# Kernel optimization log

Hardware: AMD Instinct MI355X
Metric: run time of the kernel (lower is better)

The kernel has to match this reference:

```python
import jax, jax.numpy as jnp
import numpy as np
import math

DIM = 512
HEADS = 8
DIM_HEAD = DIM // HEADS
TIME_DIM = 512
EPS = 1e-5


def _ln(x, g, b):
    m = jnp.mean(x, axis=-1, keepdims=True)
    v = jnp.var(x, axis=-1, keepdims=True)
    return (x - m) * jax.lax.rsqrt(v + EPS) * g + b


def setup_inputs() -> dict:
    key = jax.random.key(0)
    ks = jax.random.split(key, 16)
    s = 0.02
    return {
        "con_features": jax.random.normal(ks[0], (4, 1024, DIM), jnp.float32),
        "diff_features": jax.random.normal(ks[1], (4, 1024, DIM), jnp.float32),
        "time_emb": jax.random.normal(ks[2], (4, TIME_DIM), jnp.float32),
        "ln_con_g": jnp.ones((DIM,), jnp.float32),
        "ln_con_b": jnp.zeros((DIM,), jnp.float32),
        "ln_diff_g": jnp.ones((DIM,), jnp.float32),
        "ln_diff_b": jnp.zeros((DIM,), jnp.float32),
        "wq": jax.random.normal(ks[3], (DIM, DIM), jnp.float32) * s,
        "wk": jax.random.normal(ks[4], (DIM, DIM), jnp.float32) * s,
        "wv": jax.random.normal(ks[5], (DIM, DIM), jnp.float32) * s,
        "w_out": jax.random.normal(ks[6], (DIM, DIM), jnp.float32) * s,
        "b_out": jnp.zeros((DIM,), jnp.float32),
        "w_emd1": jax.random.normal(ks[7], (TIME_DIM, 2 * DIM), jnp.float32) * s,
        "b_emd1": jnp.zeros((2 * DIM,), jnp.float32),
        "w_emd2": jax.random.normal(ks[8], (2 * DIM, 2 * DIM), jnp.float32) * s,
        "b_emd2": jnp.zeros((2 * DIM,), jnp.float32),
        "mlp_ln_g": jnp.ones((DIM,), jnp.float32),
        "mlp_ln_b": jnp.zeros((DIM,), jnp.float32),
        "mlp_w1": jax.random.normal(ks[9], (DIM, DIM), jnp.float32) * s,
        "mlp_b1": jnp.zeros((DIM,), jnp.float32),
        "mlp_w2": jax.random.normal(ks[10], (DIM, DIM), jnp.float32) * s,
        "mlp_b2": jnp.zeros((DIM,), jnp.float32),
    }


def reference(con_features, diff_features, time_emb,
              ln_con_g, ln_con_b, ln_diff_g, ln_diff_b,
              wq, wk, wv, w_out, b_out,
              w_emd1, b_emd1, w_emd2, b_emd2,
              mlp_ln_g, mlp_ln_b, mlp_w1, mlp_b1, mlp_w2, mlp_b2):
    b, n, _ = diff_features.shape
    fea_q = _ln(diff_features, ln_diff_g, ln_diff_b)
    fea_kv = _ln(con_features, ln_con_g, ln_con_b)
    # projections (no bias) + split heads: b n (h d) -> b h n d
    def heads(x):
        return x.reshape(b, n, HEADS, DIM_HEAD).transpose(0, 2, 1, 3)
    q = heads(fea_q @ wq)
    k = heads(fea_kv @ wk)
    v = heads(fea_kv @ wv)
    # 2D FFT over (n, d), ortho norm
    qf = jnp.fft.fft2(q, axes=(-2, -1), norm="ortho")
    kf = jnp.fft.fft2(k, axes=(-2, -1), norm="ortho")
    dots = jnp.einsum("bhnd,bhmd->bhnm", qf, jnp.conj(kf))  # q @ k^H
    attn_c = jnp.fft.ifft2(dots, axes=(-2, -1), norm="ortho")
    mag = jnp.sqrt(attn_c.real ** 2 + attn_c.imag ** 2)
    attn = jax.nn.softmax(mag, axis=-1) / math.sqrt(DIM_HEAD)
    out = jnp.einsum("bhnm,bhmd->bhnd", attn, v)
    out = out.transpose(0, 2, 1, 3).reshape(b, n, DIM)  # b h n d -> b n (h d)
    # global per-sample normalization over (n, dim); torch.std uses ddof=1
    mu = jnp.mean(out, axis=(-2, -1), keepdims=True)
    sd = jnp.std(out, axis=(-2, -1), keepdims=True, ddof=1)
    out1 = (out - mu) / sd
    # FiLM from time embedding
    t = jax.nn.silu(time_emb @ w_emd1 + b_emd1)
    t = t @ w_emd2 + b_emd2
    mean_t, std_t = jnp.split(t, 2, axis=-1)
    out1 = out1 * std_t[:, None, :] + mean_t[:, None, :]
    out1 = out1 @ w_out + b_out
    # FeedForward: LN -> Linear -> GELU(exact) -> Linear
    h = _ln(out1, mlp_ln_g, mlp_ln_b)
    h = jax.nn.gelu(h @ mlp_w1 + mlp_b1, approximate=False)
    return h @ mlp_w2 + mlp_b2
```

## Files before the change

kernel.cpp:

```cpp
#include <hip/hip_runtime.h>
#include <math.h>


typedef _Float16 f16;
typedef _Float16 f16x4 __attribute__((ext_vector_type(4)));
typedef _Float16 f16x8 __attribute__((ext_vector_type(8)));
typedef float f32x4 __attribute__((ext_vector_type(4)));

#define ROWS 4096
#define NTOK 1024
#define NB   4
#define NH   8
#define DH   64

__device__ __forceinline__ void glds16(const f16* g, f16* l) {
    __builtin_amdgcn_global_load_lds((const __attribute__((address_space(1))) void*)g,
                                     (__attribute__((address_space(3))) void*)l, 16, 0, 0);
}

struct PrepArgs { const float* src[6]; f16* dst[6]; };

__device__ __forceinline__ void ln_row(const float* __restrict__ x, const float* __restrict__ g,
                                       const float* __restrict__ bb, f16* __restrict__ o, int lane) {
    float v[8]; float s = 0.f;
#pragma unroll
    for (int j = 0; j < 8; j++) { v[j] = x[lane + 64 * j]; s += v[j]; }
#pragma unroll
    for (int d = 32; d >= 1; d >>= 1) s += __shfl_xor(s, d, 64);
    float mean = s * (1.f / 512.f);
    float q = 0.f;
#pragma unroll
    for (int j = 0; j < 8; j++) { float t = v[j] - mean; q += t * t; }
#pragma unroll
    for (int d = 32; d >= 1; d >>= 1) q += __shfl_xor(q, d, 64);
    float inv = rsqrtf(q * (1.f / 512.f) + 1e-5f);
#pragma unroll
    for (int j = 0; j < 8; j++) {
        int c = lane + 64 * j;
        o[c] = (f16)((v[j] - mean) * inv * g[c] + bb[c]);
    }
}

__global__ __launch_bounds__(256) void k_pre(PrepArgs pa, float* statsp,
                                             const float* __restrict__ b_emd1, const float* __restrict__ b_emd2,
                                             float* __restrict__ tbacc, float* __restrict__ filmp,
                                             float* __restrict__ rstats,
                                             const float* __restrict__ diff, const float* __restrict__ g_dif,
                                             const float* __restrict__ b_dif, f16* __restrict__ A16,
                                             const float* __restrict__ con, const float* __restrict__ g_con,
                                             const float* __restrict__ b_con, f16* __restrict__ C16) {
    __shared__ float smem[1056];
    const int id = blockIdx.x, tid = threadIdx.x;
    if (id < 16) {
        int o = id * 256 + tid;
        tbacc[o] = b_emd1[o & 1023];
        filmp[o] = b_emd2[o & 1023];
        if (id < 4) statsp[id * 256 + tid] = 0.f;
    } else if (id < 48) {
        rstats[(id - 16) * 256 + tid] = 0.f;
    } else if (id < 1584) {
        int pid = id - 48;
        int m = pid >> 8, rem = pid & 255;
        int o0 = (rem & 15) * 32, i0 = (rem >> 4) * 32;
        int tx = tid & 31, ty = tid >> 5;
        const float* src = pa.src[m];
        f16* dst = pa.dst[m];
        for (int r = ty; r < 32; r += 8)
            smem[r * 33 + tx] = src[(i0 + r) * 512 + o0 + tx];
        __syncthreads();
        for (int r = ty; r < 32; r += 8)
            dst[(o0 + r) * 512 + i0 + tx] = (f16)smem[tx * 33 + r];
    } else {
        int lane = tid & 63, wid = tid >> 6;
        long row = (long)(id - 1584) * 4 + wid;
        if (row < ROWS) ln_row(diff + row * 512, g_dif, b_dif, A16 + row * 512, lane);
        else { long r = row - ROWS; ln_row(con + r * 512, g_con, b_con, C16 + r * 512, lane); }
    }
}

__global__ __launch_bounds__(256) void k_qkv(const f16* __restrict__ A16, const f16* __restrict__ C16,
                                             const f16* __restrict__ wqT, const f16* __restrict__ wkT,
                                             const f16* __restrict__ wvT,
                                             f16* __restrict__ Qh, f16* __restrict__ Kf, f16* __restrict__ Vt,
                                             const float* __restrict__ temb, const float* __restrict__ w_emd1,
                                             float* __restrict__ tbacc) {
    __shared__ __attribute__((aligned(16))) f16 sh[128 * 128 + 64 * 128];
    const int id = blockIdx.x, tid = threadIdx.x;
    if (id >= 768) {
        float* tsh = (float*)sh;
        int pid = id - 768;
        int c = (pid & 3) * 256 + tid;
        int k0 = (pid >> 2) * 32;
        if (tid < 128) tsh[(tid >> 5) * 32 + (tid & 31)] = temb[(tid >> 5) * 512 + k0 + (tid & 31)];
        __syncthreads();
        float a0 = 0.f, a1 = 0.f, a2 = 0.f, a3 = 0.f;
#pragma unroll 8
        for (int k = 0; k < 32; k++) {
            float w = w_emd1[(k0 + k) * 1024 + c];
            a0 += tsh[k] * w; a1 += tsh[32 + k] * w; a2 += tsh[64 + k] * w; a3 += tsh[96 + k] * w;
        }
        atomicAdd(&tbacc[c], a0);        atomicAdd(&tbacc[1024 + c], a1);
        atomicAdd(&tbacc[2048 + c], a2); atomicAdd(&tbacc[3072 + c], a3);
        return;
    }
    f16* Ash = sh;
    f16* Bsh = sh + 128 * 128;
    const int z = id >> 8;
    const f16* A  = (z == 0) ? A16 : C16;
    const f16* BT = (z == 0) ? wqT : (z == 1) ? wkT : wvT;
    const int lane = tid & 63, wid = tid >> 6;
    const int quad = lane >> 4, l15 = lane & 15;
    const int m0 = (id & 31) * 128, n0 = ((id >> 5) & 7) * 64;
    const int wm = (wid >> 1) * 64, wn = (wid & 1) * 32;
    const int srow = lane >> 4, slot = lane & 15;
    f32x4 acc[4][2] = {};
    for (int kk = 0; kk < 512; kk += 128) {
        if (kk) __syncthreads();
#pragma unroll
        for (int c = 0; c < 8; c++) {
            int r = c * 16 + 4 * wid + srow;
            int j = slot ^ (r & 7);
            glds16(&A[(long)(m0 + r) * 512 + kk + 8 * j], &Ash[(c * 16 + 4 * wid) * 128]);
        }
#pragma unroll
        for (int c = 0; c < 4; c++) {
            int r = c * 16 + 4 * wid + srow;
            int j = slot ^ (r & 7);
            glds16(&BT[(long)(n0 + r) * 512 + kk + 8 * j], &Bsh[(c * 16 + 4 * wid) * 128]);
        }
        __syncthreads();
#pragma unroll
        for (int ks = 0; ks < 4; ks++) {
            const int rslot = ((ks * 4 + quad) ^ (l15 & 7)) * 8;
            f16x8 af[4], bf[2];
#pragma unroll
            for (int t = 0; t < 4; t++)
                af[t] = *(const f16x8*)&Ash[(wm + t * 16 + l15) * 128 + rslot];
#pragma unroll
            for (int t = 0; t < 2; t++)
                bf[t] = *(const f16x8*)&Bsh[(wn + t * 16 + l15) * 128 + rslot];
#pragma unroll
            for (int mt = 0; mt < 4; mt++)
#pragma unroll
                for (int nt = 0; nt < 2; nt++)
                    acc[mt][nt] = __builtin_amdgcn_mfma_f32_16x16x32_f16(af[mt], bf[nt], acc[mt][nt], 0, 0, 0);
        }
    }
    __syncthreads();
    const int bb = m0 >> 10, nn0 = m0 & 1023, h = (id >> 5) & 7;
    if (z <= 1) {
#pragma unroll
        for (int mt = 0; mt < 4; mt++)
#pragma unroll
            for (int nt = 0; nt < 2; nt++)
#pragma unroll
                for (int r = 0; r < 4; r++)
                    sh[(wm + mt * 16 + quad * 4 + r) * 72 + wn + nt * 16 + l15] = (f16)acc[mt][nt][r];
        __syncthreads();
        f16* dst = (z == 0) ? Qh : Kf;
        long basebh = ((long)(bb * NH + h)) * NTOK * DH;
#pragma unroll
        for (int q2 = 0; q2 < 4; q2++) {
            int c = tid + q2 * 256;
            int row = c >> 3, col = (c & 7) * 8;
            int n = nn0 + row;
            int nr = (z == 1) ? ((NTOK - n) & (NTOK - 1)) : n;
            *(f16x8*)&dst[basebh + (long)nr * DH + col] = *(const f16x8*)&sh[row * 72 + col];
        }
    } else {
#pragma unroll
        for (int mt = 0; mt < 4; mt++)
#pragma unroll
            for (int nt = 0; nt < 2; nt++)
#pragma unroll
                for (int r = 0; r < 4; r++)
                    sh[(wn + nt * 16 + l15) * 136 + wm + mt * 16 + quad * 4 + r] = (f16)acc[mt][nt][r];
        __syncthreads();
        long basev = ((long)(bb * NH + h)) * DH * NTOK;
#pragma unroll
        for (int q2 = 0; q2 < 4; q2++) {
            int c = tid + q2 * 256;
            int d = c >> 4, col = (c & 15) * 8;
            *(f16x8*)&Vt[basev + (long)d * NTOK + nn0 + col] = *(const f16x8*)&sh[d * 136 + col];
        }
    }
}

__global__ __launch_bounds__(256) void k_attn(const f16* __restrict__ Q, const f16* __restrict__ Kf,
                                              const f16* __restrict__ Vt,
                                              float* __restrict__ Opart, float* __restrict__ lpart) {
    __shared__ __attribute__((aligned(16))) f16 Ksh[128 * 64];
    __shared__ __attribute__((aligned(16))) f16 Vsh[64 * 128];
    __shared__ __attribute__((aligned(16))) f16 PshT[4 * 16 * 136];
    const int id = blockIdx.x, tid = threadIdx.x;
    const int lane = tid & 63, wid = tid >> 6;
    const int quad = lane >> 4, l15 = lane & 15;
    const int bh = id & 31;
    const int rest = id >> 5;
    const int qt = rest & 15, half = rest >> 4;
    const int b = bh >> 3, hh = bh & 7, q0 = qt * 64;
    const int kbase = half * 512;
    const f16* Qbh = Q + (long)bh * NTOK * DH;
    const f16* Kbh = Kf + (long)bh * NTOK * DH;
    const f16* Vbh = Vt + (long)bh * DH * NTOK;
    const int rl = lane >> 3, jj8 = (lane & 7) ^ rl;
    const int rl4 = lane >> 4, jjv = (lane & 15) ^ (4 * wid + rl4);
    const int qrow = q0 + wid * 16 + l15;
    f16x8 qf[2];
    qf[0] = *(const f16x8*)&Qbh[(long)qrow * DH + quad * 8];
    qf[1] = *(const f16x8*)&Qbh[(long)qrow * DH + 32 + quad * 8];
    f32x4 O[4] = {};
    float l_acc = 0.f;
    f16* Pw = PshT + wid * 16 * 136;

    for (int k0 = 0; k0 < 512; k0 += 128) {
        if (k0) __syncthreads();
        const int kb = kbase + k0;
#pragma unroll
        for (int c = 0; c < 4; c++) {
            int rk = c * 32 + 8 * wid + rl;
            glds16(&Kbh[(long)(kb + rk) * DH + 8 * jj8], &Ksh[(c * 32 + 8 * wid) * 64]);
        }
#pragma unroll
        for (int c = 0; c < 4; c++) {
            int rv = c * 16 + 4 * wid + rl4;
            glds16(&Vbh[(long)rv * NTOK + kb + 8 * jjv], &Vsh[(c * 16 + 4 * wid) * 128]);
        }
        __syncthreads();
        f32x4 st[8] = {};
#pragma unroll
        for (int ks = 0; ks < 2; ks++) {
            const int slot = ((ks * 4 + quad) ^ (l15 & 7)) * 8;
#pragma unroll
            for (int nt = 0; nt < 8; nt++) {
                f16x8 kf = *(const f16x8*)&Ksh[(nt * 16 + l15) * 64 + slot];
                st[nt] = __builtin_amdgcn_mfma_f32_16x16x32_f16(kf, qf[ks], st[nt], 0, 0, 0);
            }
        }
#pragma unroll
        for (int nt = 0; nt < 8; nt++) {
            float p0 = __expf(fminf(fabsf(st[nt][0]) - 8.f, 11.f));
            float p1 = __expf(fminf(fabsf(st[nt][1]) - 8.f, 11.f));
            float p2 = __expf(fminf(fabsf(st[nt][2]) - 8.f, 11.f));
            float p3 = __expf(fminf(fabsf(st[nt][3]) - 8.f, 11.f));
            l_acc += (p0 + p1) + (p2 + p3);
            f16x4 pk = { (f16)p0, (f16)p1, (f16)p2, (f16)p3 };
            *(f16x4*)&Pw[l15 * 136 + 16 * nt + quad * 4] = pk;
        }
#pragma unroll
        for (int ks = 0; ks < 4; ks++) {
            f16x8 pf = *(const f16x8*)&Pw[l15 * 136 + 32 * ks + quad * 8];
            const int vslot = ((ks * 4 + quad) ^ l15) * 8;
#pragma unroll
            for (int vt = 0; vt < 4; vt++) {
                f16x8 vf = *(const f16x8*)&Vsh[(vt * 16 + l15) * 128 + vslot];
                O[vt] = __builtin_amdgcn_mfma_f32_16x16x32_f16(pf, vf, O[vt], 0, 0, 0);
            }
        }
    }
    l_acc += __shfl_xor(l_acc, 16, 64);
    l_acc += __shfl_xor(l_acc, 32, 64);
    if (quad == 0) lpart[half * (32 * NTOK) + bh * NTOK + qrow] = l_acc;
    float* Od = Opart + (size_t)half * ROWS * 512;
#pragma unroll
    for (int t = 0; t < 4; t++)
#pragma unroll
        for (int r = 0; r < 4; r++) {
            int gn = q0 + wid * 16 + quad * 4 + r;
            int gc = hh * DH + t * 16 + l15;
            Od[((long)b * NTOK + gn) * 512 + gc] = O[t][r];
        }
}

__global__ __launch_bounds__(256) void k_comb(const float* __restrict__ Opart, const float* __restrict__ lpart,
                                              f16* __restrict__ aout16, float* __restrict__ statsp,
                                              const float* __restrict__ tbacc, const float* __restrict__ w_emd2,
                                              float* __restrict__ filmp) {
    __shared__ float tsh[128];
    __shared__ float rbuf[8];
    const int id = blockIdx.x, tid = threadIdx.x;
    if (id >= 2048) {
        int pid = id - 2048;
        int c = (pid & 3) * 256 + tid;
        int k0 = (pid >> 2) * 32;
        if (tid < 128) {
            float v = tbacc[(tid >> 5) * 1024 + k0 + (tid & 31)];
            tsh[(tid >> 5) * 32 + (tid & 31)] = v / (1.f + __expf(-v));
        }
        __syncthreads();
        float a0 = 0.f, a1 = 0.f, a2 = 0.f, a3 = 0.f;
#pragma unroll 8
        for (int k = 0; k < 32; k++) {
            float w = w_emd2[(k0 + k) * 1024 + c];
            a0 += tsh[k] * w; a1 += tsh[32 + k] * w; a2 += tsh[64 + k] * w; a3 += tsh[96 + k] * w;
        }
        atomicAdd(&filmp[c], a0);        atomicAdd(&filmp[1024 + c], a1);
        atomicAdd(&filmp[2048 + c], a2); atomicAdd(&filmp[3072 + c], a3);
        return;
    }
    const int lane = tid & 63, wid = tid >> 6;
    long base = ((long)id * 256 + tid) * 4;
    int b = (int)(base >> 19);
    int row = (int)(base >> 9);
    int n = row & 1023;
    int col = (int)(base & 511);
    int h = col >> 6;
    int bhn = (b * 8 + h) * NTOK + n;
    float4 o0 = *(const float4*)&Opart[base];
    float4 o1 = *(const float4*)&Opart[(size_t)ROWS * 512 + base];
    float fr = 0.125f / (lpart[bhn] + lpart[32 * NTOK + bhn]);
    float v0 = (o0.x + o1.x) * fr, v1 = (o0.y + o1.y) * fr;
    float v2 = (o0.z + o1.z) * fr, v3 = (o0.w + o1.w) * fr;
    f16x4 pk = { (f16)v0, (f16)v1, (f16)v2, (f16)v3 };
    *(f16x4*)&aout16[base] = pk;
    float lsum = (v0 + v1) + (v2 + v3);
    float lsq = (v0 * v0 + v1 * v1) + (v2 * v2 + v3 * v3);
#pragma unroll
    for (int d = 32; d >= 1; d >>= 1) { lsum += __shfl_xor(lsum, d, 64); lsq += __shfl_xor(lsq, d, 64); }
    if (lane == 0) { rbuf[wid] = lsum; rbuf[4 + wid] = lsq; }
    __syncthreads();
    if (tid == 0) {
        float* sp = statsp + (id & 63) * 16;
        atomicAdd(&sp[b * 2], rbuf[0] + rbuf[1] + rbuf[2] + rbuf[3]);
        atomicAdd(&sp[b * 2 + 1], rbuf[4] + rbuf[5] + rbuf[6] + rbuf[7]);
    }
}

__global__ __launch_bounds__(256) void k_gemm2f(const f16* __restrict__ aout16, const float* __restrict__ statsp,
                                                const float* __restrict__ filmp,
                                                const f16* __restrict__ BT, const float* __restrict__ bias,
                                                f16* __restrict__ out1h, float* __restrict__ rstats) {
    __shared__ __attribute__((aligned(16))) f16 Ash[64 * 128];
    __shared__ __attribute__((aligned(16))) f16 Bsh[64 * 128];
    __shared__ float scsh[512], shsh[512];
    __shared__ float sred[2];
    const int tid = threadIdx.x;
    const int lane = tid & 63, wid = tid >> 6;
    const int quad = lane >> 4, l15 = lane & 15;
    const int m0 = blockIdx.x * 64, n0 = blockIdx.y * 64;
    const int wm = (wid >> 1) * 32, wn = (wid & 1) * 32;
    const int srow = lane >> 4, slot = lane & 15;
    const int b = m0 >> 10;
    if (tid < 64) {
        float s = statsp[tid * 16 + b * 2];
        float q = statsp[tid * 16 + b * 2 + 1];
#pragma unroll
        for (int d = 32; d >= 1; d >>= 1) { s += __shfl_xor(s, d, 64); q += __shfl_xor(q, d, 64); }
        if (tid == 0) { sred[0] = s; sred[1] = q; }
    }
    __syncthreads();
    {
        float sum = sred[0], sq = sred[1];
        const float M = 524288.f;
        float mu = sum / M;
        float isd = rsqrtf((sq - sum * mu) / (M - 1.f));
        for (int c = tid; c < 512; c += 256) {
            float sc = isd * filmp[b * 1024 + 512 + c];
            scsh[c] = sc;
            shsh[c] = filmp[b * 1024 + c] - mu * sc;
        }
    }
    __syncthreads();
    f32x4 acc[2][2] = {};
    for (int kk = 0; kk < 512; kk += 128) {
        if (kk) __syncthreads();
        const int j = slot ^ ((4 * wid + srow) & 7);
        const int gcol = kk + 8 * j;
        float sc[8], sf[8];
        *(float4*)&sc[0] = *(const float4*)&scsh[gcol];
        *(float4*)&sc[4] = *(const float4*)&scsh[gcol + 4];
        *(float4*)&sf[0] = *(const float4*)&shsh[gcol];
        *(float4*)&sf[4] = *(const float4*)&shsh[gcol + 4];
#pragma unroll
        for (int c = 0; c < 4; c++) {
            int r = c * 16 + 4 * wid + srow;
            f16x8 v = *(const f16x8*)&aout16[(long)(m0 + r) * 512 + gcol];
            f16x8 y;
#pragma unroll
            for (int e = 0; e < 8; e++) y[e] = (f16)((float)v[e] * sc[e] + sf[e]);
            *(f16x8*)&Ash[(c * 16 + 4 * wid) * 128 + lane * 8] = y;
            glds16(&BT[(long)(n0 + r) * 512 + kk + 8 * j], &Bsh[(c * 16 + 4 * wid) * 128]);
        }
        __syncthreads();
#pragma unroll
        for (int ks = 0; ks < 4; ks++) {
            const int rslot = ((ks * 4 + quad) ^ (l15 & 7)) * 8;
            f16x8 af[2], bf[2];
#pragma unroll
            for (int t = 0; t < 2; t++) {
                af[t] = *(const f16x8*)&Ash[(wm + t * 16 + l15) * 128 + rslot];
                bf[t] = *(const f16x8*)&Bsh[(wn + t * 16 + l15) * 128 + rslot];
            }
#pragma unroll
            for (int mt = 0; mt < 2; mt++)
#pragma unroll
                for (int nt = 0; nt < 2; nt++)
                    acc[mt][nt] = __builtin_amdgcn_mfma_f32_16x16x32_f16(af[mt], bf[nt], acc[mt][nt], 0, 0, 0);
        }
    }
#pragma unroll
    for (int mt = 0; mt < 2; mt++)
#pragma unroll
        for (int r = 0; r < 4; r++) {
            int gm = m0 + wm + mt * 16 + quad * 4 + r;
            float v0 = acc[mt][0][r] + bias[n0 + wn + l15];
            float v1 = acc[mt][1][r] + bias[n0 + wn + 16 + l15];
            out1h[(long)gm * 512 + n0 + wn + l15] = (f16)v0;
            out1h[(long)gm * 512 + n0 + wn + 16 + l15] = (f16)v1;
            float s = v0 + v1, q2 = v0 * v0 + v1 * v1;
#pragma unroll
            for (int d = 8; d >= 1; d >>= 1) { s += __shfl_xor(s, d, 16); q2 += __shfl_xor(q2, d, 16); }
            if (l15 == 0) {
                atomicAdd(&rstats[gm * 2], s);
                atomicAdd(&rstats[gm * 2 + 1], q2);
            }
        }
}

__global__ __launch_bounds__(256) void k_gemm3f(const f16* __restrict__ out1h, const float* __restrict__ rstats,
                                                const float* __restrict__ lng, const float* __restrict__ lnb,
                                                const f16* __restrict__ BT, const float* __restrict__ bias,
                                                f16* __restrict__ X4) {
    __shared__ __attribute__((aligned(16))) f16 Ash[64 * 128];
    __shared__ __attribute__((aligned(16))) f16 Bsh[64 * 128];
    __shared__ float musr[64], invsr[64], gsh[512], bsh[512];
    const int tid = threadIdx.x;
    const int lane = tid & 63, wid = tid >> 6;
    const int quad = lane >> 4, l15 = lane & 15;
    const int m0 = blockIdx.x * 64, n0 = blockIdx.y * 64;
    const int wm = (wid >> 1) * 32, wn = (wid & 1) * 32;
    const int srow = lane >> 4, slot = lane & 15;
    if (tid < 64) {
        float s = rstats[(m0 + tid) * 2], sq = rstats[(m0 + tid) * 2 + 1];
        float mu = s * (1.f / 512.f);
        float var = sq * (1.f / 512.f) - mu * mu;
        musr[tid] = mu;
        invsr[tid] = rsqrtf(var + 1e-5f);
    }
    for (int i = tid; i < 512; i += 256) { gsh[i] = lng[i]; bsh[i] = lnb[i]; }
    __syncthreads();
    f32x4 acc[2][2] = {};
    for (int kk = 0; kk < 512; kk += 128) {
        if (kk) __syncthreads();
        const int j = slot ^ ((4 * wid + srow) & 7);
        const int gcol = kk + 8 * j;
        float gv[8], bv[8];
        *(float4*)&gv[0] = *(const float4*)&gsh[gcol];
        *(float4*)&gv[4] = *(const float4*)&gsh[gcol + 4];
        *(float4*)&bv[0] = *(const float4*)&bsh[gcol];
        *(float4*)&bv[4] = *(const float4*)&bsh[gcol + 4];
#pragma unroll
        for (int c = 0; c < 4; c++) {
            int r = c * 16 + 4 * wid + srow;
            f16x8 x = *(const f16x8*)&out1h[(long)(m0 + r) * 512 + gcol];
            float a = invsr[r], m = musr[r];
            f16x8 y;
#pragma unroll
            for (int e = 0; e < 8; e++) {
                float sc = a * gv[e];
                y[e] = (f16)((float)x[e] * sc + (bv[e] - m * sc));
            }
            *(f16x8*)&Ash[(c * 16 + 4 * wid) * 128 + lane * 8] = y;
            glds16(&BT[(long)(n0 + r) * 512 + kk + 8 * j], &Bsh[(c * 16 + 4 * wid) * 128]);
        }
        __syncthreads();
#pragma unroll
        for (int ks = 0; ks < 4; ks++) {
            const int rslot = ((ks * 4 + quad) ^ (l15 & 7)) * 8;
            f16x8 af[2], bf[2];
#pragma unroll
            for (int t = 0; t < 2; t++) {
                af[t] = *(const f16x8*)&Ash[(wm + t * 16 + l15) * 128 + rslot];
                bf[t] = *(const f16x8*)&Bsh[(wn + t * 16 + l15) * 128 + rslot];
            }
#pragma unroll
            for (int mt = 0; mt < 2; mt++)
#pragma unroll
                for (int nt = 0; nt < 2; nt++)
                    acc[mt][nt] = __builtin_amdgcn_mfma_f32_16x16x32_f16(af[mt], bf[nt], acc[mt][nt], 0, 0, 0);
        }
    }
#pragma unroll
    for (int mt = 0; mt < 2; mt++)
#pragma unroll
        for (int nt = 0; nt < 2; nt++)
#pragma unroll
            for (int r = 0; r < 4; r++) {
                int gm = m0 + wm + mt * 16 + quad * 4 + r;
                int gn = n0 + wn + nt * 16 + l15;
                float x = acc[mt][nt][r] + bias[gn];
                X4[(long)gm * 512 + gn] = (f16)(0.5f * x * (1.0f + erff(x * 0.70710678f)));
            }
}

__global__ __launch_bounds__(256) void k_gemm4(const f16* __restrict__ A, const f16* __restrict__ BT,
                                               const float* __restrict__ bias, float* __restrict__ dst) {
    __shared__ __attribute__((aligned(16))) f16 Ash[64 * 128];
    __shared__ __attribute__((aligned(16))) f16 Bsh[64 * 128];
    const int tid = threadIdx.x;
    const int lane = tid & 63, wid = tid >> 6;
    const int quad = lane >> 4, l15 = lane & 15;
    const int m0 = blockIdx.x * 64, n0 = blockIdx.y * 64;
    const int wm = (wid >> 1) * 32, wn = (wid & 1) * 32;
    const int srow = lane >> 4, slot = lane & 15;
    f32x4 acc[2][2] = {};
    for (int kk = 0; kk < 512; kk += 128) {
        if (kk) __syncthreads();
#pragma unroll
        for (int c = 0; c < 4; c++) {
            int r = c * 16 + 4 * wid + srow;
            int j = slot ^ (r & 7);
            glds16(&A[(long)(m0 + r) * 512 + kk + 8 * j], &Ash[(c * 16 + 4 * wid) * 128]);
            glds16(&BT[(long)(n0 + r) * 512 + kk + 8 * j], &Bsh[(c * 16 + 4 * wid) * 128]);
        }
        __syncthreads();
#pragma unroll
        for (int ks = 0; ks < 4; ks++) {
            const int rslot = ((ks * 4 + quad) ^ (l15 & 7)) * 8;
            f16x8 af[2], bf[2];
#pragma unroll
            for (int t = 0; t < 2; t++) {
                af[t] = *(const f16x8*)&Ash[(wm + t * 16 + l15) * 128 + rslot];
                bf[t] = *(const f16x8*)&Bsh[(wn + t * 16 + l15) * 128 + rslot];
            }
#pragma unroll
            for (int mt = 0; mt < 2; mt++)
#pragma unroll
                for (int nt = 0; nt < 2; nt++)
                    acc[mt][nt] = __builtin_amdgcn_mfma_f32_16x16x32_f16(af[mt], bf[nt], acc[mt][nt], 0, 0, 0);
        }
    }
#pragma unroll
    for (int mt = 0; mt < 2; mt++)
#pragma unroll
        for (int nt = 0; nt < 2; nt++)
#pragma unroll
            for (int r = 0; r < 4; r++) {
                int gm = m0 + wm + mt * 16 + quad * 4 + r;
                int gn = n0 + wn + nt * 16 + l15;
                dst[(long)gm * 512 + gn] = acc[mt][nt][r] + bias[gn];
            }
}

extern "C" void kernel_launch(void* const* d_in, const int* in_sizes, int n_in,
                              void* d_out, int out_size, void* d_ws, size_t ws_size,
                              hipStream_t stream) {
    const float* con      = (const float*)d_in[0];
    const float* diff     = (const float*)d_in[1];
    const float* temb     = (const float*)d_in[2];
    const float* ln_con_g = (const float*)d_in[3];
    const float* ln_con_b = (const float*)d_in[4];
    const float* ln_dif_g = (const float*)d_in[5];
    const float* ln_dif_b = (const float*)d_in[6];
    const float* wq       = (const float*)d_in[7];
    const float* wk       = (const float*)d_in[8];
    const float* wv       = (const float*)d_in[9];
    const float* w_out    = (const float*)d_in[10];
    const float* b_out    = (const float*)d_in[11];
    const float* w_emd1   = (const float*)d_in[12];
    const float* b_emd1   = (const float*)d_in[13];
    const float* w_emd2   = (const float*)d_in[14];
    const float* b_emd2   = (const float*)d_in[15];
    const float* mlp_ln_g = (const float*)d_in[16];
    const float* mlp_ln_b = (const float*)d_in[17];
    const float* mlp_w1   = (const float*)d_in[18];
    const float* mlp_b1   = (const float*)d_in[19];
    const float* mlp_w2   = (const float*)d_in[20];
    const float* mlp_b2   = (const float*)d_in[21];
    float* outp = (float*)d_out;

    char* ws = (char*)d_ws;
    size_t off = 0;
    auto alloc = [&](size_t bytes) { void* p = ws + off; off += (bytes + 255) & ~(size_t)255; return p; };
    f16*   A16   = (f16*)alloc((size_t)ROWS * 512 * 2);
    f16*   C16   = (f16*)alloc((size_t)ROWS * 512 * 2);
    f16*   Qh    = (f16*)alloc((size_t)ROWS * 512 * 2);
    f16*   Kf    = (f16*)alloc((size_t)ROWS * 512 * 2);
    f16*   Vt    = (f16*)alloc((size_t)ROWS * 512 * 2);
    f16*   aout16= (f16*)alloc((size_t)ROWS * 512 * 2);
    float* Opart = (float*)alloc((size_t)2 * ROWS * 512 * 4);
    float* lpart = (float*)alloc((size_t)2 * 32 * NTOK * 4);
    f16*   wqT   = (f16*)alloc(512 * 512 * 2);
    f16*   wkT   = (f16*)alloc(512 * 512 * 2);
    f16*   wvT   = (f16*)alloc(512 * 512 * 2);
    f16*   woT   = (f16*)alloc(512 * 512 * 2);
    f16*   w1T   = (f16*)alloc(512 * 512 * 2);
    f16*   w2T   = (f16*)alloc(512 * 512 * 2);
    float* tbacc = (float*)alloc(4 * 1024 * 4);
    float* filmp = (float*)alloc(4 * 1024 * 4);
    float* statsp= (float*)alloc(64 * 16 * 4);
    float* rstats= (float*)alloc(ROWS * 2 * 4);
    f16*   out1h = Qh;
    f16*   X4    = C16;

    PrepArgs pa;
    pa.src[0] = wq;  pa.src[1] = wk;  pa.src[2] = wv;
    pa.src[3] = w_out; pa.src[4] = mlp_w1; pa.src[5] = mlp_w2;
    pa.dst[0] = wqT; pa.dst[1] = wkT; pa.dst[2] = wvT;
    pa.dst[3] = woT; pa.dst[4] = w1T; pa.dst[5] = w2T;

    k_pre<<<dim3(3632), dim3(256), 0, stream>>>(pa, statsp, b_emd1, b_emd2, tbacc, filmp, rstats,
                                                diff, ln_dif_g, ln_dif_b, A16,
                                                con, ln_con_g, ln_con_b, C16);
    k_qkv<<<dim3(832), dim3(256), 0, stream>>>(A16, C16, wqT, wkT, wvT, Qh, Kf, Vt,
                                               temb, w_emd1, tbacc);
    k_attn<<<dim3(1024), dim3(256), 0, stream>>>(Qh, Kf, Vt, Opart, lpart);
    k_comb<<<dim3(2176), dim3(256), 0, stream>>>(Opart, lpart, aout16, statsp,
                                                 tbacc, w_emd2, filmp);
    k_gemm2f<<<dim3(64, 8), dim3(256), 0, stream>>>(aout16, statsp, filmp, woT, b_out, out1h, rstats);
    k_gemm3f<<<dim3(64, 8), dim3(256), 0, stream>>>(out1h, rstats, mlp_ln_g, mlp_ln_b, w1T, mlp_b1, X4);
    k_gemm4<<<dim3(64, 8), dim3(256), 0, stream>>>(X4, w2T, mlp_b2, outp);
}
```

Baseline: 181.9 us.

## Fuse split-K attention combine into attention kernel, drop key-half split

```diff
diff --git a/kernel.cpp b/kernel.cpp
--- a/kernel.cpp
+++ b/kernel.cpp
@@ -187,19 +187,39 @@
 }
 
 __global__ __launch_bounds__(256) void k_attn(const f16* __restrict__ Q, const f16* __restrict__ Kf,
-                                              const f16* __restrict__ Vt,
-                                              float* __restrict__ Opart, float* __restrict__ lpart) {
+                                              const f16* __restrict__ Vt, f16* __restrict__ out,
+                                              float* __restrict__ statsp,
+                                              const float* __restrict__ tbacc, const float* __restrict__ w_emd2,
+                                              float* __restrict__ filmp) {
     __shared__ __attribute__((aligned(16))) f16 Ksh[128 * 64];
     __shared__ __attribute__((aligned(16))) f16 Vsh[64 * 128];
     __shared__ __attribute__((aligned(16))) f16 PshT[4 * 16 * 136];
+    __shared__ float rbuf[8];
     const int id = blockIdx.x, tid = threadIdx.x;
+    if (id >= 512) {
+        float* tsh = (float*)Ksh;
+        int pid = id - 512;
+        int c = (pid & 3) * 256 + tid;
+        int k0 = (pid >> 2) * 32;
+        if (tid < 128) {
+            float v = tbacc[(tid >> 5) * 1024 + k0 + (tid & 31)];
+            tsh[(tid >> 5) * 32 + (tid & 31)] = v / (1.f + __expf(-v));
+        }
+        __syncthreads();
+        float a0 = 0.f, a1 = 0.f, a2 = 0.f, a3 = 0.f;
+#pragma unroll 8
+        for (int k = 0; k < 32; k++) {
+            float w = w_emd2[(k0 + k) * 1024 + c];
+            a0 += tsh[k] * w; a1 += tsh[32 + k] * w; a2 += tsh[64 + k] * w; a3 += tsh[96 + k] * w;
+        }
+        atomicAdd(&filmp[c], a0);        atomicAdd(&filmp[1024 + c], a1);
+        atomicAdd(&filmp[2048 + c], a2); atomicAdd(&filmp[3072 + c], a3);
+        return;
+    }
     const int lane = tid & 63, wid = tid >> 6;
     const int quad = lane >> 4, l15 = lane & 15;
     const int bh = id & 31;
-    const int rest = id >> 5;
-    const int qt = rest & 15, half = rest >> 4;
-    const int b = bh >> 3, hh = bh & 7, q0 = qt * 64;
-    const int kbase = half * 512;
+    const int b = bh >> 3, hh = bh & 7, q0 = (id >> 5) * 64;
     const f16* Qbh = Q + (long)bh * NTOK * DH;
     const f16* Kbh = Kf + (long)bh * NTOK * DH;
     const f16* Vbh = Vt + (long)bh * DH * NTOK;
@@ -213,18 +233,17 @@
     float l_acc = 0.f;
     f16* Pw = PshT + wid * 16 * 136;
 
-    for (int k0 = 0; k0 < 512; k0 += 128) {
+    for (int k0 = 0; k0 < NTOK; k0 += 128) {
         if (k0) __syncthreads();
-        const int kb = kbase + k0;
 #pragma unroll
         for (int c = 0; c < 4; c++) {
             int rk = c * 32 + 8 * wid + rl;
-            glds16(&Kbh[(long)(kb + rk) * DH + 8 * jj8], &Ksh[(c * 32 + 8 * wid) * 64]);
+            glds16(&Kbh[(long)(k0 + rk) * DH + 8 * jj8], &Ksh[(c * 32 + 8 * wid) * 64]);
         }
 #pragma unroll
         for (int c = 0; c < 4; c++) {
             int rv = c * 16 + 4 * wid + rl4;
-            glds16(&Vbh[(long)rv * NTOK + kb + 8 * jjv], &Vsh[(c * 16 + 4 * wid) * 128]);
+            glds16(&Vbh[(long)rv * NTOK + k0 + 8 * jjv], &Vsh[(c * 16 + 4 * wid) * 128]);
         }
         __syncthreads();
         f32x4 st[8] = {};
@@ -260,61 +279,20 @@
     }
     l_acc += __shfl_xor(l_acc, 16, 64);
     l_acc += __shfl_xor(l_acc, 32, 64);
-    if (quad == 0) lpart[half * (32 * NTOK) + bh * NTOK + qrow] = l_acc;
-    float* Od = Opart + (size_t)half * ROWS * 512;
+    float lb[4];
+#pragma unroll
+    for (int r = 0; r < 4; r++) lb[r] = 0.125f / __shfl(l_acc, quad * 4 + r, 64);
+    float lsum = 0.f, lsq = 0.f;
 #pragma unroll
     for (int t = 0; t < 4; t++)
 #pragma unroll
         for (int r = 0; r < 4; r++) {
+            float v = O[t][r] * lb[r];
             int gn = q0 + wid * 16 + quad * 4 + r;
             int gc = hh * DH + t * 16 + l15;
-            Od[((long)b * NTOK + gn) * 512 + gc] = O[t][r];
-        }
-}
-
-__global__ __launch_bounds__(256) void k_comb(const float* __restrict__ Opart, const float* __restrict__ lpart,
-                                              f16* __restrict__ aout16, float* __restrict__ statsp,
-                                              const float* __restrict__ tbacc, const float* __restrict__ w_emd2,
-                                              float* __restrict__ filmp) {
-    __shared__ float tsh[128];
-    __shared__ float rbuf[8];
-    const int id = blockIdx.x, tid = threadIdx.x;
-    if (id >= 2048) {
-        int pid = id - 2048;
-        int c = (pid & 3) * 256 + tid;
-        int k0 = (pid >> 2) * 32;
-        if (tid < 128) {
-            float v = tbacc[(tid >> 5) * 1024 + k0 + (tid & 31)];
-            tsh[(tid >> 5) * 32 + (tid & 31)] = v / (1.f + __expf(-v));
-        }
-        __syncthreads();
-        float a0 = 0.f, a1 = 0.f, a2 = 0.f, a3 = 0.f;
-#pragma unroll 8
-        for (int k = 0; k < 32; k++) {
-            float w = w_emd2[(k0 + k) * 1024 + c];
-            a0 += tsh[k] * w; a1 += tsh[32 + k] * w; a2 += tsh[64 + k] * w; a3 += tsh[96 + k] * w;
-        }
-        atomicAdd(&filmp[c], a0);        atomicAdd(&filmp[1024 + c], a1);
-        atomicAdd(&filmp[2048 + c], a2); atomicAdd(&filmp[3072 + c], a3);
-        return;
-    }
-    const int lane = tid & 63, wid = tid >> 6;
-    long base = ((long)id * 256 + tid) * 4;
-    int b = (int)(base >> 19);
-    int row = (int)(base >> 9);
-    int n = row & 1023;
-    int col = (int)(base & 511);
-    int h = col >> 6;
-    int bhn = (b * 8 + h) * NTOK + n;
-    float4 o0 = *(const float4*)&Opart[base];
-    float4 o1 = *(const float4*)&Opart[(size_t)ROWS * 512 + base];
-    float fr = 0.125f / (lpart[bhn] + lpart[32 * NTOK + bhn]);
-    float v0 = (o0.x + o1.x) * fr, v1 = (o0.y + o1.y) * fr;
-    float v2 = (o0.z + o1.z) * fr, v3 = (o0.w + o1.w) * fr;
-    f16x4 pk = { (f16)v0, (f16)v1, (f16)v2, (f16)v3 };
-    *(f16x4*)&aout16[base] = pk;
-    float lsum = (v0 + v1) + (v2 + v3);
-    float lsq = (v0 * v0 + v1 * v1) + (v2 * v2 + v3 * v3);
+            out[((long)b * NTOK + gn) * 512 + gc] = (f16)v;
+            lsum += v; lsq += v * v;
+        }
 #pragma unroll
     for (int d = 32; d >= 1; d >>= 1) { lsum += __shfl_xor(lsum, d, 64); lsq += __shfl_xor(lsq, d, 64); }
     if (lane == 0) { rbuf[wid] = lsum; rbuf[4 + wid] = lsq; }
@@ -578,8 +556,6 @@
     f16*   Kf    = (f16*)alloc((size_t)ROWS * 512 * 2);
     f16*   Vt    = (f16*)alloc((size_t)ROWS * 512 * 2);
     f16*   aout16= (f16*)alloc((size_t)ROWS * 512 * 2);
-    float* Opart = (float*)alloc((size_t)2 * ROWS * 512 * 4);
-    float* lpart = (float*)alloc((size_t)2 * 32 * NTOK * 4);
     f16*   wqT   = (f16*)alloc(512 * 512 * 2);
     f16*   wkT   = (f16*)alloc(512 * 512 * 2);
     f16*   wvT   = (f16*)alloc(512 * 512 * 2);
@@ -604,9 +580,8 @@
                                                 con, ln_con_g, ln_con_b, C16);
     k_qkv<<<dim3(832), dim3(256), 0, stream>>>(A16, C16, wqT, wkT, wvT, Qh, Kf, Vt,
                                                temb, w_emd1, tbacc);
-    k_attn<<<dim3(1024), dim3(256), 0, stream>>>(Qh, Kf, Vt, Opart, lpart);
-    k_comb<<<dim3(2176), dim3(256), 0, stream>>>(Opart, lpart, aout16, statsp,
-                                                 tbacc, w_emd2, filmp);
+    k_attn<<<dim3(640), dim3(256), 0, stream>>>(Qh, Kf, Vt, aout16, statsp,
+                                                tbacc, w_emd2, filmp);
     k_gemm2f<<<dim3(64, 8), dim3(256), 0, stream>>>(aout16, statsp, filmp, woT, b_out, out1h, rstats);
     k_gemm3f<<<dim3(64, 8), dim3(256), 0, stream>>>(out1h, rstats, mlp_ln_g, mlp_ln_b, w1T, mlp_b1, X4);
     k_gemm4<<<dim3(64, 8), dim3(256), 0, stream>>>(X4, w2T, mlp_b2, outp);
```

Result: faster. 177.9 us (-2.2%).
